# Optimization experiments

Measured on AMD Instinct MI355X. Metric: run time of the kernel, lower is better.

Reference implementation:

```python
import jax, jax.numpy as jnp
import numpy as np

D = 512
B, S1, S2 = 8, 2048, 2048


def setup_inputs() -> dict:
    key = jax.random.key(0)
    ks = jax.random.split(key, 8)
    s = 1.0 / np.sqrt(D)
    return {
        "x1": jax.random.normal(ks[0], (B, S1, D), dtype=jnp.float32),
        "x2": jax.random.normal(ks[1], (B, S2, D), dtype=jnp.float32),
        "Wq": jax.random.normal(ks[2], (D, D), dtype=jnp.float32) * s,
        "bq": jnp.zeros((D,), dtype=jnp.float32),
        "Wk": jax.random.normal(ks[3], (D, D), dtype=jnp.float32) * s,
        "bk": jnp.zeros((D,), dtype=jnp.float32),
        "Wv": jax.random.normal(ks[4], (D, D), dtype=jnp.float32) * s,
        "bv": jnp.zeros((D,), dtype=jnp.float32),
    }


def reference(x1, x2, Wq, bq, Wk, bk, Wv, bv):
    # q,k,v projections (torch Linear: x @ W^T + b)
    q = jnp.einsum("bsd,ed->bse", x1, Wq) + bq  # [B,S1,D]
    k = jnp.einsum("btd,ed->bte", x2, Wk) + bk  # [B,S2,D]
    v = jnp.einsum("btd,ed->bte", x2, Wv) + bv  # [B,S2,D]
    # NOTE: source scales by input_dim (D), not sqrt(D)
    scores = jnp.einsum("bse,bte->bst", q, k) / D  # [B,S1,S2]
    attn = jax.nn.softmax(scores, axis=-1)
    return jnp.einsum("bst,bte->bse", attn, v)  # [B,S1,D]
```

## Files before the change

### kernel.cpp

```cpp
#include <hip/hip_runtime.h>

using u8  = unsigned char;
using u16 = unsigned short;
using u32 = unsigned int;
using s16x8 = __attribute__((ext_vector_type(8))) short;
using bf16x8 = __attribute__((ext_vector_type(8))) __bf16;
using f32x4 = __attribute__((ext_vector_type(4))) float;
using i32x4 = __attribute__((ext_vector_type(4))) int;
using i32x8 = __attribute__((ext_vector_type(8))) int;

__device__ inline u16 f2bf(float f) {
  u32 u = __float_as_uint(f);
  u = (u + 0x7FFFu + ((u >> 16) & 1u)) >> 16;
  return (u16)u;
}

__device__ inline u8 f2fp8(float f) {
  return (u8)(__builtin_amdgcn_cvt_pk_fp8_f32(f, f, 0, false) & 0xFF);
}

__device__ inline f32x4 mfma16(s16x8 a, s16x8 b, f32x4 c) {
  return __builtin_amdgcn_mfma_f32_16x16x32_bf16(
      __builtin_bit_cast(bf16x8, a), __builtin_bit_cast(bf16x8, b), c, 0, 0, 0);
}

__device__ inline f32x4 mfma_fp8(i32x8 a, i32x8 b, f32x4 c) {
  return __builtin_amdgcn_mfma_scale_f32_16x16x128_f8f6f4(
      a, b, c, 0 , 0 , 0, 127, 0, 127);
}

__device__ inline void load_lds16(const void* g, void* l) {
  __builtin_amdgcn_global_load_lds(
      (const __attribute__((address_space(1))) void*)g,
      (__attribute__((address_space(3))) void*)l, 16, 0, 0);
}

__global__ __launch_bounds__(256) void cast_x12(
    const float* __restrict__ x1, const float* __restrict__ x2,
    u16* __restrict__ o1, u16* __restrict__ o2) {
  const float* in = blockIdx.y ? x2 : x1;
  u16* out = blockIdx.y ? o2 : o1;
  int i = (blockIdx.x * 256 + threadIdx.x) * 4;
  float4 f = *(const float4*)(in + i);
  ushort4 o;
  o.x = f2bf(f.x); o.y = f2bf(f.y); o.z = f2bf(f.z); o.w = f2bf(f.w);
  *(ushort4*)(out + i) = o;
}

__global__ __launch_bounds__(256) void cast_w3z(
    const float* __restrict__ a, const float* __restrict__ b,
    const float* __restrict__ c, u16* __restrict__ oa, u16* __restrict__ ob,
    u16* __restrict__ oc) {
  const float* in = blockIdx.y == 0 ? a : (blockIdx.y == 1 ? b : c);
  u16* out = blockIdx.y == 0 ? oa : (blockIdx.y == 1 ? ob : oc);
  int i = (blockIdx.x * 256 + threadIdx.x) * 4;
  float4 f = *(const float4*)(in + i);
  ushort4 o;
  o.x = f2bf(f.x); o.y = f2bf(f.y); o.z = f2bf(f.z); o.w = f2bf(f.w);
  *(ushort4*)(out + i) = o;
}

template <int EPI>
__global__ __launch_bounds__(256) void gemm64(
    const u16* __restrict__ A, const u16* __restrict__ B,
    const u16* __restrict__ B2, void* __restrict__ C, void* __restrict__ C2,
    const float* __restrict__ bias, const float* __restrict__ bias2,
    int M, int N, int K, long sA, long sB, long sC) {
  const int bz = blockIdx.z;
  const int nwg = gridDim.x * gridDim.y;
  int flat = blockIdx.x + gridDim.x * blockIdx.y;
  flat = (flat & 7) * (nwg >> 3) + (flat >> 3);
  const int m0 = (flat / gridDim.x) * 128;
  const int n0 = (flat % gridDim.x) * 128;
  const u16* Ab = A + (size_t)bz * sA;
  const u16* Bsel = (EPI == 4 && n0 >= 512) ? B2 : B;
  const int nb = (EPI == 4 && n0 >= 512) ? n0 - 512 : n0;
  const u16* Bb = Bsel + (size_t)bz * sB;
  const int tid = threadIdx.x;
  const int lane = tid & 63;
  const int wave = tid >> 6;
  const int wm = (wave >> 1) * 64;
  const int wn = (wave & 1) * 64;

  __shared__ u16 SM[128 * 64 * 2];
  u16* As = SM;
  u16* Bs = SM + 128 * 64;

  const int sr = lane >> 3;
  const int gd = (lane & 7) ^ sr;
  const int ch0 = wave * 4;

  f32x4 acc[4][4];
#pragma unroll
  for (int i = 0; i < 4; ++i)
#pragma unroll
    for (int j = 0; j < 4; ++j) acc[i][j] = 0.0f;

  const int fr = lane & 15;
  const int fg = lane >> 4;

  for (int k0 = 0; k0 < K; k0 += 64) {
#pragma unroll
    for (int it = 0; it < 4; ++it) {
      const int ch = ch0 + it;
      const int row = ch * 8 + sr;
      load_lds16(Ab + (size_t)(m0 + row) * K + k0 + gd * 8, &As[ch * 512]);
      load_lds16(Bb + (size_t)(nb + row) * K + k0 + gd * 8, &Bs[ch * 512]);
    }
    __syncthreads();
#pragma unroll
    for (int s = 0; s < 2; ++s) {
      const int slot = ((s * 4 + fg) ^ (fr & 7)) * 8;
      s16x8 af[4], bfr[4];
#pragma unroll
      for (int i = 0; i < 4; ++i) {
        af[i]  = *(const s16x8*)&As[(wm + i * 16 + fr) * 64 + slot];
        bfr[i] = *(const s16x8*)&Bs[(wn + i * 16 + fr) * 64 + slot];
      }
#pragma unroll
      for (int mi = 0; mi < 4; ++mi)
#pragma unroll
        for (int ni = 0; ni < 4; ++ni)
          acc[mi][ni] = mfma16(af[mi], bfr[ni], acc[mi][ni]);
    }
    __syncthreads();
  }

  const int er = fg * 4;
  const int ec = fr;

  if (EPI == 0) {
    u8* Cb = (u8*)C;
#pragma unroll
    for (int mi = 0; mi < 4; ++mi)
#pragma unroll
      for (int ni = 0; ni < 4; ++ni) {
        const int col = n0 + wn + ni * 16 + ec;
        const float badd = bias[col];
#pragma unroll
        for (int i = 0; i < 4; ++i) {
          const int row = m0 + wm + mi * 16 + er + i;
          Cb[(size_t)row * N + col] = f2fp8(acc[mi][ni][i] + badd);
        }
      }
  } else {
    if (n0 < 512) {
      u8* Cb = (u8*)C;
#pragma unroll
      for (int mi = 0; mi < 4; ++mi)
#pragma unroll
        for (int ni = 0; ni < 4; ++ni) {
          const int col = n0 + wn + ni * 16 + ec;
          const float badd = bias[col];
#pragma unroll
          for (int i = 0; i < 4; ++i) {
            const int row = m0 + wm + mi * 16 + er + i;
            Cb[(size_t)row * 512 + col] = f2fp8(acc[mi][ni][i] + badd);
          }
        }
    } else {
      u16* Tb = SM;
      const int batch = m0 >> 11;
      const int srow = m0 & 2047;
      u16* Cv = (u16*)C2 + (size_t)batch * (512 * 2048);
#pragma unroll
      for (int h = 0; h < 2; ++h) {
        if ((wn >> 6) == h) {
#pragma unroll
          for (int mi = 0; mi < 4; ++mi)
#pragma unroll
            for (int ni = 0; ni < 4; ++ni) {
              const int c = ni * 16 + ec;
              const float badd = bias2[n0 - 512 + wn + c];
#pragma unroll
              for (int i = 0; i < 4; ++i) {
                const int r = wm + mi * 16 + er + i;
                Tb[c * 136 + r] = f2bf(acc[mi][ni][i] + badd);
              }
            }
        }
        __syncthreads();
        const int d = tid >> 2;
        const int sc = (tid & 3) * 32;
        const int dglob = n0 - 512 + 64 * h + d;
#pragma unroll
        for (int j = 0; j < 4; ++j) {
          uint4 v = *(const uint4*)&Tb[d * 136 + sc + j * 8];
          *(uint4*)&Cv[(size_t)dglob * 2048 + srow + sc + j * 8] = v;
        }
        __syncthreads();
      }
    }
  }
}

__global__ __launch_bounds__(512, 2) void attn_fused(
    const u8* __restrict__ q8, const u8* __restrict__ k8,
    const u16* __restrict__ vT, float* __restrict__ out) {
  const int batch = blockIdx.x;
  const int q0 = blockIdx.y * 64;
  const u8* qb = q8 + ((size_t)batch * 2048 + q0) * 512;
  const u8* kb = k8 + (size_t)batch * 2048 * 512;
  const u16* vb = vT + (size_t)batch * 512 * 2048;
  float* ob = out + ((size_t)batch * 2048 + q0) * 512;

  const int tid = threadIdx.x;
  const int lane = tid & 63;
  const int wave = tid >> 6;
  const int wm = (wave >> 2) * 32;
  const int wn = (wave & 3) * 32;
  const int sr = lane >> 3;
  const int gd = (lane & 7) ^ sr;
  const int fr = lane & 15;
  const int fg = lane >> 4;
  const int r7 = fr & 7;
  const int s0 = (2 * fg) ^ r7;
  const int s1 = s0 ^ 1;

  __shared__ u8 Ks[4][16384];
  __shared__ u16 Ps[64 * 128];
  __shared__ float l_lds[64];
  if (tid < 64) l_lds[tid] = 0.0f;

  i32x8 Qf[2][4];
#pragma unroll
  for (int mi = 0; mi < 2; ++mi)
#pragma unroll
    for (int kc = 0; kc < 4; ++kc) {
      const u8* p = qb + (size_t)(wm + mi * 16 + fr) * 512 + kc * 128 + fg * 32;
      i32x4 lo = *(const i32x4*)p;
      i32x4 hi = *(const i32x4*)(p + 16);
      i32x8 q;
      q[0] = lo[0]; q[1] = lo[1]; q[2] = lo[2]; q[3] = lo[3];
      q[4] = hi[0]; q[5] = hi[1]; q[6] = hi[2]; q[7] = hi[3];
      Qf[mi][kc] = q;
    }

#pragma unroll
  for (int it = 0; it < 8; ++it) {
    const int idx = wave * 8 + it;
    const int kc = idx >> 4, sub = idx & 15;
    load_lds16(kb + (size_t)(sub * 8 + sr) * 512 + kc * 128 + gd * 16,
               &Ks[kc][sub * 1024]);
  }
  __syncthreads();

  f32x4 oacc[4][4];
#pragma unroll
  for (int i = 0; i < 4; ++i)
#pragma unroll
    for (int j = 0; j < 4; ++j) oacc[i][j] = 0.0f;
  float l_reg[2][4] = {{0.0f, 0.0f, 0.0f, 0.0f}, {0.0f, 0.0f, 0.0f, 0.0f}};

  for (int t = 0; t < 16; ++t) {
    const int kv0 = t * 128;

    f32x4 sacc[2][2];
#pragma unroll
    for (int i = 0; i < 2; ++i)
#pragma unroll
      for (int j = 0; j < 2; ++j) sacc[i][j] = 0.0f;
#pragma unroll
    for (int kc = 0; kc < 4; ++kc) {
      i32x8 bf2[2];
#pragma unroll
      for (int ni = 0; ni < 2; ++ni) {
        const u8* pb = &Ks[kc][(wn + ni * 16 + fr) * 128];
        i32x4 blo = *(const i32x4*)(pb + s0 * 16);
        i32x4 bhi = *(const i32x4*)(pb + s1 * 16);
        i32x8 b;
        b[0] = blo[0]; b[1] = blo[1]; b[2] = blo[2]; b[3] = blo[3];
        b[4] = bhi[0]; b[5] = bhi[1]; b[6] = bhi[2]; b[7] = bhi[3];
        bf2[ni] = b;
      }
#pragma unroll
      for (int mi = 0; mi < 2; ++mi)
#pragma unroll
        for (int ni = 0; ni < 2; ++ni)
          sacc[mi][ni] = mfma_fp8(Qf[mi][kc], bf2[ni], sacc[mi][ni]);
    }

#pragma unroll
    for (int mi = 0; mi < 2; ++mi)
#pragma unroll
      for (int ni = 0; ni < 2; ++ni) {
        const int c = wn + ni * 16 + fr;
        const int g = c >> 3;
        const int co = c & 7;
#pragma unroll
        for (int i = 0; i < 4; ++i) {
          const int r = wm + mi * 16 + fg * 4 + i;
          const float p = __expf(sacc[mi][ni][i] * (1.0f / 512.0f));
          Ps[r * 128 + ((g ^ (r & 7)) << 3) + co] = f2bf(p);
          l_reg[mi][i] += p;
        }
      }
    __syncthreads();

    if (t < 15) {
#pragma unroll
      for (int it = 0; it < 8; ++it) {
        const int idx = wave * 8 + it;
        const int kc = idx >> 4, sub = idx & 15;
        load_lds16(
            kb + (size_t)(kv0 + 128 + sub * 8 + sr) * 512 + kc * 128 + gd * 16,
            &Ks[kc][sub * 1024]);
      }
    }

#pragma unroll
    for (int ks = 0; ks < 4; ++ks) {
      s16x8 pa[4];
#pragma unroll
      for (int mi = 0; mi < 4; ++mi) {
        const int r = mi * 16 + fr;
        pa[mi] = *(const s16x8*)&Ps[r * 128 + (((ks * 4 + fg) ^ (r & 7)) << 3)];
      }
#pragma unroll
      for (int ni = 0; ni < 4; ++ni) {
        const int d = wave * 64 + ni * 16 + fr;
        const s16x8 bv =
            *(const s16x8*)&vb[(size_t)d * 2048 + kv0 + ks * 32 + fg * 8];
#pragma unroll
        for (int mi = 0; mi < 4; ++mi)
          oacc[mi][ni] = mfma16(pa[mi], bv, oacc[mi][ni]);
      }
    }
    __syncthreads();
  }

#pragma unroll
  for (int mi = 0; mi < 2; ++mi)
#pragma unroll
    for (int i = 0; i < 4; ++i) {
      float rs = l_reg[mi][i];
      rs += __shfl_xor(rs, 1);
      rs += __shfl_xor(rs, 2);
      rs += __shfl_xor(rs, 4);
      rs += __shfl_xor(rs, 8);
      if (fr == 0) atomicAdd(&l_lds[wm + mi * 16 + fg * 4 + i], rs);
    }
  __syncthreads();

#pragma unroll
  for (int mi = 0; mi < 4; ++mi)
#pragma unroll
    for (int i = 0; i < 4; ++i) {
      const int r = mi * 16 + fg * 4 + i;
      const float li = __builtin_amdgcn_rcpf(l_lds[r]);
#pragma unroll
      for (int ni = 0; ni < 4; ++ni)
        ob[(size_t)r * 512 + wave * 64 + ni * 16 + fr] = oacc[mi][ni][i] * li;
    }
}

extern "C" void kernel_launch(void* const* d_in, const int* in_sizes, int n_in,
                              void* d_out, int out_size, void* d_ws, size_t ws_size,
                              hipStream_t stream) {
  constexpr int B = 8, S = 2048, D = 512;
  constexpr size_t MS = (size_t)B * S;

  const float* x1 = (const float*)d_in[0];
  const float* x2 = (const float*)d_in[1];
  const float* Wq = (const float*)d_in[2];
  const float* bq = (const float*)d_in[3];
  const float* Wk = (const float*)d_in[4];
  const float* bk = (const float*)d_in[5];
  const float* Wv = (const float*)d_in[6];
  const float* bv = (const float*)d_in[7];
  float* out = (float*)d_out;

  u16* x1b = (u16*)d_ws;
  u16* x2b = x1b + MS * D;
  u16* Wqb = x2b + MS * D;
  u16* Wkb = Wqb + (size_t)D * D;
  u16* Wvb = Wkb + (size_t)D * D;
  u16* vTb = Wvb + (size_t)D * D;
  u16* Sc  = vTb + MS * D;
  float* lbuf = (float*)(Sc + (size_t)B * S * S);
  u8* qb8 = (u8*)(lbuf + MS);
  u8* kb8 = qb8 + MS * D;

  dim3 blk(256);

  cast_x12<<<dim3((MS * D) / 1024, 2), blk, 0, stream>>>(x1, x2, x1b, x2b);
  cast_w3z<<<dim3((D * D) / 1024, 3), blk, 0, stream>>>(
      Wq, Wk, Wv, Wqb, Wkb, Wvb);

  gemm64<0><<<dim3(4, 128, 1), blk, 0, stream>>>(
      x1b, Wqb, nullptr, qb8, nullptr, bq, nullptr,
      16384, 512, 512, 0, 0, 0);

  gemm64<4><<<dim3(8, 128, 1), blk, 0, stream>>>(
      x2b, Wkb, Wvb, kb8, vTb, bk, bv,
      16384, 512, 512, 0, 0, 0);

  attn_fused<<<dim3(8, 32, 1), dim3(512), 0, stream>>>(qb8, kb8, vTb, out);
}
```

Baseline: 272.3 us.

## Double-buffer K and P tiles with register-prefetched V in fused attention

Shrinks the KV tile from 128 to 64 keys and double-buffers the K tile and P matrix in LDS, so each iteration needs one barrier instead of two. The K tile two steps ahead is staged asynchronously, and the V fragments for the next tile are prefetched into registers while the current P·V MFMAs run. Row-sum reduction switches from LDS atomics to per-wave partial sums stored in reused LDS and added at the end. The aim is to hide global-memory latency for K and V behind compute. The cost is more registers for the V prefetch and twice as many smaller tiles.

Result: slower. 332.4 us (+22.1%).

```diff
diff --git a/kernel.cpp b/kernel.cpp
--- a/kernel.cpp
+++ b/kernel.cpp
@@ -208,7 +208,8 @@
   const int lane = tid & 63;
   const int wave = tid >> 6;
   const int wm = (wave >> 2) * 32;
-  const int wn = (wave & 3) * 32;
+  const int wn = (wave & 3) * 16;
+  const int wd = wave * 64;
   const int sr = lane >> 3;
   const int gd = (lane & 7) ^ sr;
   const int fr = lane & 15;
@@ -217,10 +218,8 @@
   const int s0 = (2 * fg) ^ r7;
   const int s1 = s0 ^ 1;
 
-  __shared__ u8 Ks[4][16384];
-  __shared__ u16 Ps[64 * 128];
-  __shared__ float l_lds[64];
-  if (tid < 64) l_lds[tid] = 0.0f;
+  __shared__ u8 Ks[2][4][8192];
+  __shared__ u16 Ps[2][64 * 64];
 
   i32x8 Qf[2][4];
 #pragma unroll
@@ -236,14 +235,23 @@
       Qf[mi][kc] = q;
     }
 
-#pragma unroll
-  for (int it = 0; it < 8; ++it) {
-    const int idx = wave * 8 + it;
-    const int kc = idx >> 4, sub = idx & 15;
-    load_lds16(kb + (size_t)(sub * 8 + sr) * 512 + kc * 128 + gd * 16,
-               &Ks[kc][sub * 1024]);
-  }
-  __syncthreads();
+  auto stageK = [&](int kv0, int buf) {
+#pragma unroll
+    for (int it = 0; it < 4; ++it) {
+      const int idx = wave * 4 + it;
+      const int kc = idx >> 3, sub = idx & 7;
+      load_lds16(kb + (size_t)(kv0 + sub * 8 + sr) * 512 + kc * 128 + gd * 16,
+                 &Ks[buf][kc][sub * 1024]);
+    }
+  };
+  auto loadV = [&](int kv0, s16x8* Vr) {
+#pragma unroll
+    for (int ks = 0; ks < 2; ++ks)
+#pragma unroll
+      for (int ni = 0; ni < 4; ++ni)
+        Vr[ks * 4 + ni] = *(const s16x8*)&vb[(size_t)(wd + ni * 16 + fr) * 2048 +
+                                             kv0 + ks * 32 + fg * 8];
+  };
 
   f32x4 oacc[4][4];
 #pragma unroll
@@ -252,83 +260,67 @@
     for (int j = 0; j < 4; ++j) oacc[i][j] = 0.0f;
   float l_reg[2][4] = {{0.0f, 0.0f, 0.0f, 0.0f}, {0.0f, 0.0f, 0.0f, 0.0f}};
 
-  for (int t = 0; t < 16; ++t) {
-    const int kv0 = t * 128;
-
-    f32x4 sacc[2][2];
-#pragma unroll
-    for (int i = 0; i < 2; ++i)
-#pragma unroll
-      for (int j = 0; j < 2; ++j) sacc[i][j] = 0.0f;
+  s16x8 Vr0[8], Vr1[8];
+
+  constexpr int NT = 32;
+
+  auto tile = [&](int t, int psel, const s16x8* Vcur, s16x8* Vnxt) {
+    f32x4 sacc[2];
+    sacc[0] = 0.0f; sacc[1] = 0.0f;
 #pragma unroll
     for (int kc = 0; kc < 4; ++kc) {
-      i32x8 bf2[2];
-#pragma unroll
-      for (int ni = 0; ni < 2; ++ni) {
-        const u8* pb = &Ks[kc][(wn + ni * 16 + fr) * 128];
-        i32x4 blo = *(const i32x4*)(pb + s0 * 16);
-        i32x4 bhi = *(const i32x4*)(pb + s1 * 16);
-        i32x8 b;
-        b[0] = blo[0]; b[1] = blo[1]; b[2] = blo[2]; b[3] = blo[3];
-        b[4] = bhi[0]; b[5] = bhi[1]; b[6] = bhi[2]; b[7] = bhi[3];
-        bf2[ni] = b;
-      }
+      const u8* pb = &Ks[psel][kc][(wn + fr) * 128];
+      i32x4 blo = *(const i32x4*)(pb + s0 * 16);
+      i32x4 bhi = *(const i32x4*)(pb + s1 * 16);
+      i32x8 bK;
+      bK[0] = blo[0]; bK[1] = blo[1]; bK[2] = blo[2]; bK[3] = blo[3];
+      bK[4] = bhi[0]; bK[5] = bhi[1]; bK[6] = bhi[2]; bK[7] = bhi[3];
 #pragma unroll
       for (int mi = 0; mi < 2; ++mi)
-#pragma unroll
-        for (int ni = 0; ni < 2; ++ni)
-          sacc[mi][ni] = mfma_fp8(Qf[mi][kc], bf2[ni], sacc[mi][ni]);
-    }
-
+        sacc[mi] = mfma_fp8(Qf[mi][kc], bK, sacc[mi]);
+    }
+    u16* Pd = &Ps[psel][0];
+    const int g = (wn >> 3) + (fr >> 3);
 #pragma unroll
     for (int mi = 0; mi < 2; ++mi)
 #pragma unroll
-      for (int ni = 0; ni < 2; ++ni) {
-        const int c = wn + ni * 16 + fr;
-        const int g = c >> 3;
-        const int co = c & 7;
-#pragma unroll
-        for (int i = 0; i < 4; ++i) {
-          const int r = wm + mi * 16 + fg * 4 + i;
-          const float p = __expf(sacc[mi][ni][i] * (1.0f / 512.0f));
-          Ps[r * 128 + ((g ^ (r & 7)) << 3) + co] = f2bf(p);
-          l_reg[mi][i] += p;
-        }
+      for (int i = 0; i < 4; ++i) {
+        const int r = wm + mi * 16 + fg * 4 + i;
+        const float p = __expf(sacc[mi][i] * (1.0f / 512.0f));
+        l_reg[mi][i] += p;
+        Pd[r * 64 + ((g ^ (r & 7)) << 3) + (fr & 7)] = f2bf(p);
       }
     __syncthreads();
-
-    if (t < 15) {
-#pragma unroll
-      for (int it = 0; it < 8; ++it) {
-        const int idx = wave * 8 + it;
-        const int kc = idx >> 4, sub = idx & 15;
-        load_lds16(
-            kb + (size_t)(kv0 + 128 + sub * 8 + sr) * 512 + kc * 128 + gd * 16,
-            &Ks[kc][sub * 1024]);
-      }
-    }
-
-#pragma unroll
-    for (int ks = 0; ks < 4; ++ks) {
+    if (t + 2 < NT) stageK((t + 2) * 64, psel);
+    if (t + 1 < NT) loadV((t + 1) * 64, Vnxt);
+#pragma unroll
+    for (int ks = 0; ks < 2; ++ks) {
       s16x8 pa[4];
 #pragma unroll
       for (int mi = 0; mi < 4; ++mi) {
         const int r = mi * 16 + fr;
-        pa[mi] = *(const s16x8*)&Ps[r * 128 + (((ks * 4 + fg) ^ (r & 7)) << 3)];
-      }
-#pragma unroll
-      for (int ni = 0; ni < 4; ++ni) {
-        const int d = wave * 64 + ni * 16 + fr;
-        const s16x8 bv =
-            *(const s16x8*)&vb[(size_t)d * 2048 + kv0 + ks * 32 + fg * 8];
+        pa[mi] = *(const s16x8*)&Pd[r * 64 + (((ks * 4 + fg) ^ (r & 7)) << 3)];
+      }
+#pragma unroll
+      for (int ni = 0; ni < 4; ++ni)
 #pragma unroll
         for (int mi = 0; mi < 4; ++mi)
-          oacc[mi][ni] = mfma16(pa[mi], bv, oacc[mi][ni]);
-      }
-    }
-    __syncthreads();
+          oacc[mi][ni] = mfma16(pa[mi], Vcur[ks * 4 + ni], oacc[mi][ni]);
+    }
+  };
+
+  stageK(0, 0);
+  loadV(0, Vr0);
+  __syncthreads();
+  stageK(64, 1);
+
+  for (int tt = 0; tt < NT; tt += 2) {
+    tile(tt, 0, Vr0, Vr1);
+    tile(tt + 1, 1, Vr1, Vr0);
   }
 
+  float* lsc = (float*)&Ps[0][0];
+  __syncthreads();
 #pragma unroll
   for (int mi = 0; mi < 2; ++mi)
 #pragma unroll
@@ -338,7 +330,7 @@
       rs += __shfl_xor(rs, 2);
       rs += __shfl_xor(rs, 4);
       rs += __shfl_xor(rs, 8);
-      if (fr == 0) atomicAdd(&l_lds[wm + mi * 16 + fg * 4 + i], rs);
+      if (fr == 0) lsc[(wn >> 4) * 64 + wm + mi * 16 + fg * 4 + i] = rs;
     }
   __syncthreads();
 
@@ -347,10 +339,11 @@
 #pragma unroll
     for (int i = 0; i < 4; ++i) {
       const int r = mi * 16 + fg * 4 + i;
-      const float li = __builtin_amdgcn_rcpf(l_lds[r]);
+      const float l = lsc[r] + lsc[64 + r] + lsc[128 + r] + lsc[192 + r];
+      const float li = __builtin_amdgcn_rcpf(l);
 #pragma unroll
       for (int ni = 0; ni < 4; ++ni)
-        ob[(size_t)r * 512 + wave * 64 + ni * 16 + fr] = oacc[mi][ni][i] * li;
+        ob[(size_t)r * 512 + wd + ni * 16 + fr] = oacc[mi][ni][i] * li;
     }
 }
 
```
